# Kernel tuning notes

Measured on AMD Instinct MI355X. Metric: run time of the kernel, lower is better.

Reference implementation:

```python
import jax, jax.numpy as jnp
import numpy as np

B, S = 64, 256
VOCAB = 2048          # input_size == num_keys
EMB = 256             # emb_dimension
HID = 1024            # hidden_size


def setup_inputs() -> dict:
    key = jax.random.key(0)
    ks = jax.random.split(key, 12)
    s = lambda fan_in: 1.0 / np.sqrt(fan_in)
    return {
        "x": jax.random.randint(ks[0], (B, S), 0, VOCAB, dtype=jnp.int32),
        "emb": jax.random.uniform(ks[1], (VOCAB, EMB), jnp.float32, -0.05, 0.05),
        # layer-1 LSTM: input EMB -> HID, gates order (i, f, g, o)
        "W1": jax.random.normal(ks[2], (EMB, 4 * HID), jnp.float32) * s(EMB),
        "U1": jax.random.normal(ks[3], (HID, 4 * HID), jnp.float32) * s(HID),
        "b1": jnp.zeros((4 * HID,), jnp.float32),
        # layer-2 LSTM: input HID -> HID
        "W2": jax.random.normal(ks[4], (HID, 4 * HID), jnp.float32) * s(HID),
        "U2": jax.random.normal(ks[5], (HID, 4 * HID), jnp.float32) * s(HID),
        "b2": jnp.zeros((4 * HID,), jnp.float32),
        "Wd1": jax.random.normal(ks[6], (HID, HID), jnp.float32) * s(HID),
        "bd1": jnp.zeros((HID,), jnp.float32),
        "Wd2": jax.random.normal(ks[7], (HID, VOCAB), jnp.float32) * s(HID),
        "bd2": jnp.zeros((VOCAB,), jnp.float32),
    }


def _lstm_cell(x_t, h, c, W, U, b):
    # Keras LSTMCell: gates in order i, f, g(cell), o
    z = x_t @ W + h @ U + b                     # [B, 4H]
    i, f, g, o = jnp.split(z, 4, axis=-1)
    i, f, o = jax.nn.sigmoid(i), jax.nn.sigmoid(f), jax.nn.sigmoid(o)
    c_new = f * c + i * jnp.tanh(g)
    h_new = o * jnp.tanh(c_new)
    return h_new, c_new


def _stacked_lstm(inputs, mask, W1, U1, b1, W2, U2, b2):
    # inputs: [B, S, EMB]; mask: [B, S] bool (mask_zero semantics)
    xs = (jnp.swapaxes(inputs, 0, 1), jnp.swapaxes(mask, 0, 1))  # time-major
    Bsz = inputs.shape[0]
    z = jnp.zeros((Bsz, HID), inputs.dtype)
    init = (z, z, z, z, z)  # h1, c1, h2, c2, prev_out

    def step(carry, inp):
        h1, c1, h2, c2, prev_out = carry
        x_t, m_t = inp
        m = m_t[:, None]
        h1n, c1n = _lstm_cell(x_t, h1, c1, W1, U1, b1)
        h2n, c2n = _lstm_cell(h1n, h2, c2, W2, U2, b2)
        # Keras RNN masking: carry old state / previous output at masked steps
        h1n = jnp.where(m, h1n, h1)
        c1n = jnp.where(m, c1n, c1)
        h2n = jnp.where(m, h2n, h2)
        c2n = jnp.where(m, c2n, c2)
        out = jnp.where(m, h2n, prev_out)
        return (h1n, c1n, h2n, c2n, out), out

    _, seq = jax.lax.scan(step, init, xs)       # [S, B, HID]
    return jnp.swapaxes(seq, 0, 1)              # [B, S, HID]


def reference(x, emb, W1, U1, b1, W2, U2, b2, Wd1, bd1, Wd2, bd2):
    inputs = emb[x]                              # [B, S, EMB]
    mask = x != 0                                # mask_zero=True
    seq = _stacked_lstm(inputs, mask, W1, U1, b1, W2, U2, b2)
    h = jax.nn.sigmoid(seq @ Wd1 + bd1)          # dense1, sigmoid
    out = jax.nn.sigmoid(h @ Wd2 + bd2)          # dense2, sigmoid -> [B, S, VOCAB]
    return out
```

## Files before the change

### kernel.cpp

```cpp
#include <hip/hip_runtime.h>
#include <hip/hip_bf16.h>


#define DI __device__ __forceinline__

typedef __attribute__((ext_vector_type(8))) short s8v;
typedef __attribute__((ext_vector_type(4))) float f4v;

DI f4v mfma16(s8v a, s8v b, f4v c){
  return __builtin_amdgcn_mfma_f32_16x16x32_bf16(a, b, c, 0, 0, 0);
}
DI s8v as_s8(uint4 u){ return __builtin_bit_cast(s8v, u); }

DI unsigned short f2b(float f){
  unsigned u = __float_as_uint(f);
  u = u + 0x7fffu + ((u >> 16) & 1u);
  return (unsigned short)(u >> 16);
}
DI float b2f(unsigned short h){ return __uint_as_float(((unsigned)h) << 16); }
DI float sig_(float x){ return 1.f / (1.f + __expf(-x)); }
DI float tanh_(float x){ return 1.f - 2.f / (__expf(2.f * x) + 1.f); }

DI uint4 ldA(const unsigned long long* p){
  unsigned long long lo = __hip_atomic_load(p,     __ATOMIC_RELAXED, __HIP_MEMORY_SCOPE_AGENT);
  unsigned long long hi = __hip_atomic_load(p + 1, __ATOMIC_RELAXED, __HIP_MEMORY_SCOPE_AGENT);
  uint4 r; r.x = (unsigned)lo; r.y = (unsigned)(lo >> 32);
  r.z = (unsigned)hi; r.w = (unsigned)(hi >> 32);
  return r;
}
DI unsigned short ldH(const unsigned short* p){
  return __hip_atomic_load(p, __ATOMIC_RELAXED, __HIP_MEMORY_SCOPE_AGENT);
}
DI void stH(unsigned short* p, unsigned short v){
  __hip_atomic_store(p, v, __ATOMIC_RELAXED, __HIP_MEMORY_SCOPE_AGENT);
}

__global__ __launch_bounds__(256) void k_pack_AB(const float* __restrict__ Wx,
                                                 const float* __restrict__ Ux,
                                                 unsigned short* __restrict__ dst,
                                                 int KS, int kx){
  int idx = blockIdx.x * 256 + threadIdx.x;
  if (idx >= 256 * KS * 64) return;
  int l = idx & 63, rest = idx >> 6;
  int ks = rest % KS, b = rest / KS;
  int c = l & 15;
  int col = 4 * b + (c & 3) + ((c >> 2) << 10);
  int k0 = ks * 32 + ((l >> 4) << 3);
  const float* src = (k0 < kx) ? (Wx + (size_t)k0 * 4096)
                               : (Ux + (size_t)(k0 - kx) * 4096);
  unsigned v[4];
  #pragma unroll
  for (int p = 0; p < 4; ++p){
    unsigned short lo = f2b(src[(size_t)(2 * p) * 4096 + col]);
    unsigned short hi = f2b(src[(size_t)(2 * p + 1) * 4096 + col]);
    v[p] = (unsigned)lo | ((unsigned)hi << 16);
  }
  uint4 o; o.x = v[0]; o.y = v[1]; o.z = v[2]; o.w = v[3];
  ((uint4*)dst)[idx] = o;
}

__global__ __launch_bounds__(256) void k_pack_D(const float* __restrict__ W,
                                                unsigned short* __restrict__ dst,
                                                int CG, int N){
  int idx = blockIdx.x * 256 + threadIdx.x;
  if (idx >= CG * 32 * 64) return;
  int l = idx & 63;
  int ks = (idx >> 6) & 31;
  int cg = idx >> 11;
  int col = 16 * cg + (l & 15);
  int k0 = 32 * ks + ((l >> 4) << 3);
  unsigned v[4];
  #pragma unroll
  for (int p = 0; p < 4; ++p){
    unsigned short lo = f2b(W[(size_t)(k0 + 2 * p) * N + col]);
    unsigned short hi = f2b(W[(size_t)(k0 + 2 * p + 1) * N + col]);
    v[p] = (unsigned)lo | ((unsigned)hi << 16);
  }
  uint4 o; o.x = v[0]; o.y = v[1]; o.z = v[2]; o.w = v[3];
  ((uint4*)dst)[idx] = o;
}

__global__ __launch_bounds__(256) void k_embed(const int* __restrict__ x,
                                               const float* __restrict__ emb,
                                               unsigned short* __restrict__ dst){
  int idx = blockIdx.x * 256 + threadIdx.x;
  int l = idx & 63;
  int w = (idx >> 6) & 3;
  int ks = (idx >> 8) & 7;
  int t = idx >> 11;
  int row = 16 * w + (l & 15);
  int xi = x[row * 256 + t];
  int k0 = 32 * ks + ((l >> 4) << 3);
  const float* src = emb + (size_t)xi * 256 + k0;
  unsigned v[4];
  #pragma unroll
  for (int p = 0; p < 4; ++p){
    unsigned short lo = f2b(src[2 * p]);
    unsigned short hi = f2b(src[2 * p + 1]);
    v[p] = (unsigned)lo | ((unsigned)hi << 16);
  }
  uint4 o; o.x = v[0]; o.y = v[1]; o.z = v[2]; o.w = v[3];
  ((uint4*)dst)[idx] = o;
}

__global__ __launch_bounds__(512, 2) void k_scan(
    const unsigned short* __restrict__ esw,
    const unsigned short* __restrict__ WA,
    const unsigned short* __restrict__ WB,
    const float* __restrict__ b1v, const float* __restrict__ b2v,
    const int* __restrict__ x,
    unsigned short* __restrict__ h1b, unsigned short* __restrict__ h2b,
    float* __restrict__ c1, float* __restrict__ c2,
    unsigned short* __restrict__ seq, float* __restrict__ zpart,
    int* __restrict__ bar){
  __shared__ uint4 Blds[2][64][64];
  const int blk = blockIdx.x, tid = threadIdx.x;
  const int w = tid >> 6, l = tid & 63;
  const bool isL2 = (blk >= 128);
  const int bk = isL2 ? blk - 128 : blk;
  const int kh = w >> 2, rt = w & 3;
  const int c = l & 15, u = c & 3, g = c >> 2;
  const uint4* WAu  = (const uint4*)WA;
  const uint4* WBu  = (const uint4*)WB;
  const uint4* eswU = (const uint4*)esw;

  if (!isL2){
    for (int i = tid; i < 5120; i += 512){
      int ct = (i >= 2560) ? 1 : 0;
      int r = ct ? i - 2560 : i;
      Blds[ct][r >> 6][r & 63] = WAu[((size_t)(2 * bk + ct) * 40 + (r >> 6)) * 64 + (r & 63)];
    }
  } else {
    for (int i = tid; i < 8192; i += 512){
      int ct = i >> 12;
      int r = i & 4095;
      Blds[ct][r >> 6][r & 63] = WBu[((size_t)(2 * bk + ct) * 64 + (r >> 6)) * 64 + (r & 63)];
    }
  }
  __syncthreads();

  #pragma unroll 1
  for (int p = 0; p <= 256; ++p){
    const int par = p & 1;
    const bool active = isL2 ? (p >= 1) : (p < 256);
    f4v acc0 = {0.f, 0.f, 0.f, 0.f};
    f4v acc1 = {0.f, 0.f, 0.f, 0.f};

    if (!isL2){
      if (active){
        const unsigned long long* h1p =
            (const unsigned long long*)(h1b + (size_t)par * 65536);
        if (kh == 0){
          uint4 a[20];
          const uint4* eswT = eswU + (size_t)p * 2048;
          #pragma unroll
          for (int j = 0; j < 8; ++j)
            a[j] = eswT[(j * 4 + rt) * 64 + l];
          #pragma unroll
          for (int j = 0; j < 12; ++j)
            a[8 + j] = ldA(h1p + (size_t)((j * 4 + rt) * 64 + l) * 2);
          #pragma unroll
          for (int j = 0; j < 20; ++j){
            acc0 = mfma16(as_s8(a[j]), as_s8(Blds[0][j][l]), acc0);
            acc1 = mfma16(as_s8(a[j]), as_s8(Blds[1][j][l]), acc1);
          }
        } else {
          uint4 a[20];
          #pragma unroll
          for (int j = 0; j < 20; ++j)
            a[j] = ldA(h1p + (size_t)(((j + 12) * 4 + rt) * 64 + l) * 2);
          #pragma unroll
          for (int j = 0; j < 20; ++j){
            acc0 = mfma16(as_s8(a[j]), as_s8(Blds[0][20 + j][l]), acc0);
            acc1 = mfma16(as_s8(a[j]), as_s8(Blds[1][20 + j][l]), acc1);
          }
        }
      }
    } else {
      if (active){
        const unsigned long long* hp = (const unsigned long long*)
            ((kh ? h2b : h1b) + (size_t)par * 65536);
        uint4 a[32];
        #pragma unroll
        for (int j = 0; j < 32; ++j)
          a[j] = ldA(hp + (size_t)((j * 4 + rt) * 64 + l) * 2);
        const int kb = kh * 32;
        #pragma unroll
        for (int j = 0; j < 32; ++j){
          acc0 = mfma16(as_s8(a[j]), as_s8(Blds[0][kb + j][l]), acc0);
          acc1 = mfma16(as_s8(a[j]), as_s8(Blds[1][kb + j][l]), acc1);
        }
      }
    }

    f4v* zp = (f4v*)zpart;
    const size_t zbase = ((size_t)blk * 4 + rt) * 2;
    if (kh == 1){
      zp[(zbase + 0) * 64 + l] = acc0;
      zp[(zbase + 1) * 64 + l] = acc1;
    }
    __syncthreads();

    if (kh == 0 && active){
      acc0 += zp[(zbase + 0) * 64 + l];
      acc1 += zp[(zbase + 1) * 64 + l];

      const int t = isL2 ? (p - 1) : p;
      float* cc = isL2 ? c2 : c1;
      const float* bb = isL2 ? b2v : b1v;
      const unsigned short* hin  = (isL2 ? h2b : h1b) + (size_t)par * 65536;
      unsigned short*       hout = (isL2 ? h2b : h1b) + (size_t)(par ^ 1) * 65536;

      #pragma unroll
      for (int ct = 0; ct < 2; ++ct){
        f4v z = ct ? acc1 : acc0;
        const int ug = 8 * bk + 4 * ct + u;
        const float bv = bb[ug + (g << 10)];
        #pragma unroll
        for (int q = 0; q < 4; ++q){
          float zb = z[q] + bv;
          float a1 = __shfl_xor(zb, 4);
          float a2 = __shfl_xor(zb, 8);
          float a3 = __shfl_xor(zb, 12);
          float v0 = zb, v1 = a1, v2 = a2, v3 = a3;
          if (g & 1){ float s = v0; v0 = v1; v1 = s; s = v2; v2 = v3; v3 = s; }
          if (g & 2){ float s = v0; v0 = v2; v2 = s; s = v1; v1 = v3; v3 = s; }
          const int row = 16 * rt + ((l >> 4) << 2) + q;
          float cold = cc[row * 1024 + ug];
          float iv = sig_(v0), fv = sig_(v1), gv = tanh_(v2), ov = sig_(v3);
          float cn = fv * cold + iv * gv;
          float hn = ov * tanh_(cn);
          const int fidx = (((ug >> 5) * 4 + (row >> 4)) * 64 + (row & 15)
                            + (((ug >> 3) & 3) << 4)) * 8 + (ug & 7);
          const bool m = (x[row * 256 + t] != 0);
          if (!isL2){
            if (!m){ cn = cold; hn = b2f(ldH(hin + fidx)); }
            if (g == 0)      stH(hout + fidx, f2b(hn));
            else if (g == 1) cc[row * 1024 + ug] = cn;
          } else {
            float prev = (t > 0)
                ? b2f(seq[((size_t)row * 256 + (t - 1)) * 1024 + ug]) : 0.f;
            float outv = hn;
            if (!m){ cn = cold; hn = b2f(ldH(hin + fidx)); outv = prev; }
            if (g == 0)      stH(hout + fidx, f2b(hn));
            else if (g == 1) cc[row * 1024 + ug] = cn;
            else if (g == 2) seq[((size_t)row * 256 + t) * 1024 + ug] = f2b(outv);
          }
        }
      }
    }

    if (p < 256){
      __syncthreads();
      if (tid == 0){
        int v = __hip_atomic_fetch_add(bar + (blk >> 5) * 64, 1,
                                       __ATOMIC_RELAXED, __HIP_MEMORY_SCOPE_AGENT);
        if (v == 32 * (p + 1) - 1)
          __hip_atomic_fetch_add(bar + 512, 1,
                                 __ATOMIC_RELAXED, __HIP_MEMORY_SCOPE_AGENT);
        const int target = 8 * (p + 1);
        while (__hip_atomic_load(bar + 512, __ATOMIC_RELAXED,
                                 __HIP_MEMORY_SCOPE_AGENT) < target)
          __builtin_amdgcn_s_sleep(2);
      }
      __syncthreads();
    }
  }
}

__global__ __launch_bounds__(256) void k_dec(const unsigned short* __restrict__ A,
                                             const unsigned short* __restrict__ WF,
                                             const float* __restrict__ bias,
                                             void* __restrict__ outp,
                                             int N, int wf32){
  const int nb = N >> 7;
  const int rm = blockIdx.x / nb, cn = blockIdx.x - rm * nb;
  const int w = threadIdx.x >> 6, l = threadIdx.x & 63;
  const int r0 = rm * 128 + (w >> 1) * 64;
  const int c0 = cn * 128 + (w & 1) * 64;
  f4v acc[4][4];
  #pragma unroll
  for (int i = 0; i < 4; ++i)
    #pragma unroll
    for (int j = 0; j < 4; ++j) acc[i][j] = (f4v){0.f, 0.f, 0.f, 0.f};

  const uint4* WFu = (const uint4*)WF;
  #pragma unroll 4
  for (int ks = 0; ks < 32; ++ks){
    uint4 a4[4], b4[4];
    #pragma unroll
    for (int i = 0; i < 4; ++i)
      a4[i] = *(const uint4*)(A + (size_t)(r0 + 16 * i + (l & 15)) * 1024 + ks * 32 + ((l >> 4) << 3));
    #pragma unroll
    for (int j = 0; j < 4; ++j)
      b4[j] = WFu[(((c0 >> 4) + j) * 32 + ks) * 64 + l];
    #pragma unroll
    for (int i = 0; i < 4; ++i)
      #pragma unroll
      for (int j = 0; j < 4; ++j)
        acc[i][j] = mfma16(as_s8(a4[i]), as_s8(b4[j]), acc[i][j]);
  }
  #pragma unroll
  for (int j = 0; j < 4; ++j){
    const int col = c0 + 16 * j + (l & 15);
    const float bv = bias[col];
    #pragma unroll
    for (int i = 0; i < 4; ++i){
      #pragma unroll
      for (int q = 0; q < 4; ++q){
        const int row = r0 + 16 * i + ((l >> 4) << 2) + q;
        float v = sig_(acc[i][j][q] + bv);
        if (wf32) ((float*)outp)[(size_t)row * N + col] = v;
        else      ((unsigned short*)outp)[(size_t)row * N + col] = f2b(v);
      }
    }
  }
}

extern "C" void kernel_launch(void* const* d_in, const int* in_sizes, int n_in,
                              void* d_out, int out_size, void* d_ws, size_t ws_size,
                              hipStream_t stream){
  const int*   x    = (const int*)  d_in[0];
  const float* emb  = (const float*)d_in[1];
  const float* W1   = (const float*)d_in[2];
  const float* U1   = (const float*)d_in[3];
  const float* b1   = (const float*)d_in[4];
  const float* W2   = (const float*)d_in[5];
  const float* U2   = (const float*)d_in[6];
  const float* b2   = (const float*)d_in[7];
  const float* Wd1  = (const float*)d_in[8];
  const float* bd1  = (const float*)d_in[9];
  const float* Wd2  = (const float*)d_in[10];
  const float* bd2  = (const float*)d_in[11];

  char* ws = (char*)d_ws;
  unsigned short* WA   = (unsigned short*)(ws + 0);
  unsigned short* WB   = (unsigned short*)(ws + 10485760);
  unsigned short* Wd1F = (unsigned short*)(ws + 27262976);
  unsigned short* Wd2F = (unsigned short*)(ws + 29360128);
  unsigned short* esw  = (unsigned short*)(ws + 33554432);
  unsigned short* h1b  = (unsigned short*)(ws + 41943040);
  unsigned short* h2b  = (unsigned short*)(ws + 42205184);
  float*          c1   = (float*)        (ws + 42467328);
  float*          c2   = (float*)        (ws + 42729472);
  unsigned short* seq  = (unsigned short*)(ws + 42991616);
  unsigned short* hd   = (unsigned short*)(ws + 76546048);
  int*            bar  = (int*)          (ws + 110100480);
  float*          zpart = (float*)hd;
  (void)in_sizes; (void)n_in; (void)out_size; (void)ws_size;

  k_pack_AB<<<2560, 256, 0, stream>>>(W1, U1, WA, 40, 256);
  k_pack_AB<<<4096, 256, 0, stream>>>(W2, U2, WB, 64, 1024);
  k_pack_D <<<512,  256, 0, stream>>>(Wd1, Wd1F, 64, 1024);
  k_pack_D <<<1024, 256, 0, stream>>>(Wd2, Wd2F, 128, 2048);
  k_embed  <<<2048, 256, 0, stream>>>(x, emb, esw);
  hipMemsetAsync(ws + 41943040, 0, 1048576, stream);
  hipMemsetAsync(ws + 110100480, 0, 4096, stream);

  k_scan<<<256, 512, 0, stream>>>(esw, WA, WB, b1, b2, x,
                                  h1b, h2b, c1, c2, seq, zpart, bar);

  k_dec<<<1024, 256, 0, stream>>>(seq, Wd1F, bd1, hd,    1024, 0);
  k_dec<<<2048, 256, 0, stream>>>(hd,  Wd2F, bd2, d_out, 2048, 1);
}
```

Before: 4.213 ms.

## Use 32-slot rotating hidden-state ring so h loads become plain cached reads

Replaces the double-buffered h1/h2 state with a 32-deep ring buffer indexed by step, so each step reads a fresh address never seen before. This lets the recurrent-state loads drop from 64-bit relaxed atomics to plain 128-bit vector loads, relying on address freshness to avoid stale cache hits instead of atomic semantics. It saves load instructions and latency on the critical sequential scan path. The risk is coherence: a non-atomic load could still hit a stale line if it was cached from 32 steps earlier, and the ring uses more workspace memory.

```diff
diff --git a/kernel.cpp b/kernel.cpp
--- a/kernel.cpp
+++ b/kernel.cpp
@@ -21,16 +21,6 @@
 DI float sig_(float x){ return 1.f / (1.f + __expf(-x)); }
 DI float tanh_(float x){ return 1.f - 2.f / (__expf(2.f * x) + 1.f); }
 
-DI uint4 ldA(const unsigned long long* p){
-  unsigned long long lo = __hip_atomic_load(p,     __ATOMIC_RELAXED, __HIP_MEMORY_SCOPE_AGENT);
-  unsigned long long hi = __hip_atomic_load(p + 1, __ATOMIC_RELAXED, __HIP_MEMORY_SCOPE_AGENT);
-  uint4 r; r.x = (unsigned)lo; r.y = (unsigned)(lo >> 32);
-  r.z = (unsigned)hi; r.w = (unsigned)(hi >> 32);
-  return r;
-}
-DI unsigned short ldH(const unsigned short* p){
-  return __hip_atomic_load(p, __ATOMIC_RELAXED, __HIP_MEMORY_SCOPE_AGENT);
-}
 DI void stH(unsigned short* p, unsigned short v){
   __hip_atomic_store(p, v, __ATOMIC_RELAXED, __HIP_MEMORY_SCOPE_AGENT);
 }
@@ -109,7 +99,7 @@
     const unsigned short* __restrict__ WB,
     const float* __restrict__ b1v, const float* __restrict__ b2v,
     const int* __restrict__ x,
-    unsigned short* __restrict__ h1b, unsigned short* __restrict__ h2b,
+    unsigned short* __restrict__ h1r, unsigned short* __restrict__ h2r,
     float* __restrict__ c1, float* __restrict__ c2,
     unsigned short* __restrict__ seq, float* __restrict__ zpart,
     int* __restrict__ bar){
@@ -141,15 +131,14 @@
 
   #pragma unroll 1
   for (int p = 0; p <= 256; ++p){
-    const int par = p & 1;
     const bool active = isL2 ? (p >= 1) : (p < 256);
+    const uint4* h1i = (const uint4*)(h1r + (size_t)(p & 31) * 65536);
+    const uint4* h2i = (const uint4*)(h2r + (size_t)(p & 31) * 65536);
     f4v acc0 = {0.f, 0.f, 0.f, 0.f};
     f4v acc1 = {0.f, 0.f, 0.f, 0.f};
 
     if (!isL2){
       if (active){
-        const unsigned long long* h1p =
-            (const unsigned long long*)(h1b + (size_t)par * 65536);
         if (kh == 0){
           uint4 a[20];
           const uint4* eswT = eswU + (size_t)p * 2048;
@@ -158,7 +147,7 @@
             a[j] = eswT[(j * 4 + rt) * 64 + l];
           #pragma unroll
           for (int j = 0; j < 12; ++j)
-            a[8 + j] = ldA(h1p + (size_t)((j * 4 + rt) * 64 + l) * 2);
+            a[8 + j] = h1i[(j * 4 + rt) * 64 + l];
           #pragma unroll
           for (int j = 0; j < 20; ++j){
             acc0 = mfma16(as_s8(a[j]), as_s8(Blds[0][j][l]), acc0);
@@ -168,7 +157,7 @@
           uint4 a[20];
           #pragma unroll
           for (int j = 0; j < 20; ++j)
-            a[j] = ldA(h1p + (size_t)(((j + 12) * 4 + rt) * 64 + l) * 2);
+            a[j] = h1i[((j + 12) * 4 + rt) * 64 + l];
           #pragma unroll
           for (int j = 0; j < 20; ++j){
             acc0 = mfma16(as_s8(a[j]), as_s8(Blds[0][20 + j][l]), acc0);
@@ -178,12 +167,11 @@
       }
     } else {
       if (active){
-        const unsigned long long* hp = (const unsigned long long*)
-            ((kh ? h2b : h1b) + (size_t)par * 65536);
+        const uint4* hp = kh ? h2i : h1i;
         uint4 a[32];
         #pragma unroll
         for (int j = 0; j < 32; ++j)
-          a[j] = ldA(hp + (size_t)((j * 4 + rt) * 64 + l) * 2);
+          a[j] = hp[(j * 4 + rt) * 64 + l];
         const int kb = kh * 32;
         #pragma unroll
         for (int j = 0; j < 32; ++j){
@@ -208,8 +196,8 @@
       const int t = isL2 ? (p - 1) : p;
       float* cc = isL2 ? c2 : c1;
       const float* bb = isL2 ? b2v : b1v;
-      const unsigned short* hin  = (isL2 ? h2b : h1b) + (size_t)par * 65536;
-      unsigned short*       hout = (isL2 ? h2b : h1b) + (size_t)(par ^ 1) * 65536;
+      const unsigned short* hin  = (isL2 ? h2r : h1r) + (size_t)(p & 31) * 65536;
+      unsigned short*       hout = (isL2 ? h2r : h1r) + (size_t)((p + 1) & 31) * 65536;
 
       #pragma unroll
       for (int ct = 0; ct < 2; ++ct){
@@ -234,14 +222,14 @@
                             + (((ug >> 3) & 3) << 4)) * 8 + (ug & 7);
           const bool m = (x[row * 256 + t] != 0);
           if (!isL2){
-            if (!m){ cn = cold; hn = b2f(ldH(hin + fidx)); }
+            if (!m){ cn = cold; hn = b2f(hin[fidx]); }
             if (g == 0)      stH(hout + fidx, f2b(hn));
             else if (g == 1) cc[row * 1024 + ug] = cn;
           } else {
             float prev = (t > 0)
                 ? b2f(seq[((size_t)row * 256 + (t - 1)) * 1024 + ug]) : 0.f;
             float outv = hn;
-            if (!m){ cn = cold; hn = b2f(ldH(hin + fidx)); outv = prev; }
+            if (!m){ cn = cold; hn = b2f(hin[fidx]); outv = prev; }
             if (g == 0)      stH(hout + fidx, f2b(hn));
             else if (g == 1) cc[row * 1024 + ug] = cn;
             else if (g == 2) seq[((size_t)row * 256 + t) * 1024 + ug] = f2b(outv);
@@ -339,14 +327,14 @@
   unsigned short* Wd1F = (unsigned short*)(ws + 27262976);
   unsigned short* Wd2F = (unsigned short*)(ws + 29360128);
   unsigned short* esw  = (unsigned short*)(ws + 33554432);
-  unsigned short* h1b  = (unsigned short*)(ws + 41943040);
-  unsigned short* h2b  = (unsigned short*)(ws + 42205184);
   float*          c1   = (float*)        (ws + 42467328);
   float*          c2   = (float*)        (ws + 42729472);
   unsigned short* seq  = (unsigned short*)(ws + 42991616);
   unsigned short* hd   = (unsigned short*)(ws + 76546048);
   int*            bar  = (int*)          (ws + 110100480);
-  float*          zpart = (float*)hd;
+  float*          zpart = (float*)(ws + 76546048);
+  unsigned short* h1r  = (unsigned short*)(ws + 78643200);
+  unsigned short* h2r  = (unsigned short*)(ws + 82837504);
   (void)in_sizes; (void)n_in; (void)out_size; (void)ws_size;
 
   k_pack_AB<<<2560, 256, 0, stream>>>(W1, U1, WA, 40, 256);
@@ -354,11 +342,13 @@
   k_pack_D <<<512,  256, 0, stream>>>(Wd1, Wd1F, 64, 1024);
   k_pack_D <<<1024, 256, 0, stream>>>(Wd2, Wd2F, 128, 2048);
   k_embed  <<<2048, 256, 0, stream>>>(x, emb, esw);
-  hipMemsetAsync(ws + 41943040, 0, 1048576, stream);
+  hipMemsetAsync(ws + 42467328, 0, 524288, stream);
+  hipMemsetAsync(ws + 78643200, 0, 131072, stream);
+  hipMemsetAsync(ws + 82837504, 0, 131072, stream);
   hipMemsetAsync(ws + 110100480, 0, 4096, stream);
 
   k_scan<<<256, 512, 0, stream>>>(esw, WA, WB, b1, b2, x,
-                                  h1b, h2b, c1, c2, seq, zpart, bar);
+                                  h1r, h2r, c1, c2, seq, zpart, bar);
 
   k_dec<<<1024, 256, 0, stream>>>(seq, Wd1F, bd1, hd,    1024, 0);
   k_dec<<<2048, 256, 0, stream>>>(hd,  Wd2F, bd2, d_out, 2048, 1);
```

After: 3.919 ms. 1.07x faster.
